# Kernel optimization log

Measured on AMD Instinct MI355X. Metric: run time of the kernel, lower is better.

The kernel has to match this reference:

```python
import jax, jax.numpy as jnp
import numpy as np

B, T, C, H = 4, 2048, 1024, 16
D = C // H  # head_dim = 64


def setup_inputs() -> dict:
    key = jax.random.key(0)
    ks = jax.random.split(key, 5)
    s = 0.02
    return {
        "x": jax.random.normal(ks[0], (B, T, C), dtype=jnp.float32),
        "w_qkv": jax.random.normal(ks[1], (C, 3 * C), dtype=jnp.float32) * s,
        "b_qkv": jnp.zeros((3 * C,), dtype=jnp.float32),
        "w_proj": jax.random.normal(ks[2], (C, C), dtype=jnp.float32) * s,
        "b_proj": jnp.zeros((C,), dtype=jnp.float32),
    }


def reference(x, w_qkv, b_qkv, w_proj, b_proj):
    Bx, Tx, Cx = x.shape
    qkv = x @ w_qkv + b_qkv                      # [B,T,3C]
    q, k, v = jnp.split(qkv, 3, axis=-1)
    # [B,T,C] -> [B,H,T,D]
    q = q.reshape(Bx, Tx, H, D).transpose(0, 2, 1, 3)
    k = k.reshape(Bx, Tx, H, D).transpose(0, 2, 1, 3)
    v = v.reshape(Bx, Tx, H, D).transpose(0, 2, 1, 3)
    scale = 1.0 / np.sqrt(D).astype(np.float32)
    attn = jnp.einsum('bhqd,bhkd->bhqk', q, k) * scale   # [B,H,T,T]
    causal = jnp.tril(jnp.ones((Tx, Tx), dtype=bool))
    attn = jnp.where(causal[None, None], attn, -jnp.inf)
    attn = jax.nn.softmax(attn, axis=-1)
    out = jnp.einsum('bhqk,bhkd->bhqd', attn, v)          # [B,H,T,D]
    out = out.transpose(0, 2, 1, 3).reshape(Bx, Tx, Cx)   # [B,T,C]
    return out @ w_proj + b_proj
```

## Files before the change

kernel.cpp:

```cpp
#include <hip/hip_runtime.h>
#include <hip/hip_bf16.h>
#include <math.h>

using bf16 = __hip_bfloat16;
typedef __bf16 bf16x8 __attribute__((ext_vector_type(8)));
typedef float  f32x4  __attribute__((ext_vector_type(4)));
typedef unsigned short ushort8 __attribute__((ext_vector_type(8)));

#define DEV __device__ __forceinline__

DEV void gld_lds16(const void* g, void* l) {
    __builtin_amdgcn_global_load_lds((const __attribute__((address_space(1))) void*)g,
                                     (__attribute__((address_space(3))) void*)l,
                                     16, 0, 0);
}

__global__ __launch_bounds__(256) void cast_f32_bf16(const float* __restrict__ in,
                                                     bf16* __restrict__ out, int n4) {
    int i = blockIdx.x * blockDim.x + threadIdx.x;
    if (i >= n4) return;
    float4 f = ((const float4*)in)[i];
    __align__(8) bf16 o[4] = {__float2bfloat16(f.x), __float2bfloat16(f.y),
                              __float2bfloat16(f.z), __float2bfloat16(f.w)};
    ((uint64_t*)out)[i] = *(const uint64_t*)o;
}

__global__ __launch_bounds__(256) void transpose_cast(const float* __restrict__ in,
                                                      bf16* __restrict__ out, int R, int Cn) {
    __shared__ float tile[32][33];
    int bx = blockIdx.x * 32;
    int by = blockIdx.y * 32;
    int tx = threadIdx.x & 31, ty = threadIdx.x >> 5;
    for (int i = ty; i < 32; i += 8)
        tile[i][tx] = in[(size_t)(by + i) * Cn + bx + tx];
    __syncthreads();
    for (int i = ty; i < 32; i += 8)
        out[(size_t)(bx + i) * R + by + tx] = __float2bfloat16(tile[tx][i]);
}

__global__ __launch_bounds__(256) void gemm_qkv(const bf16* __restrict__ A,
                                                const bf16* __restrict__ Bt,
                                                const float* __restrict__ bias,
                                                bf16* __restrict__ qb,
                                                bf16* __restrict__ kb,
                                                bf16* __restrict__ vTb) {
    constexpr int K = 1024, T = 2048;
    constexpr float CS = 0.18033688f;
    __shared__ __align__(16) bf16 Al[128 * 32];
    __shared__ __align__(16) bf16 Bl[128 * 32];
    __shared__ __align__(16) bf16 Et[32 * 136];
    int tid = threadIdx.x;
    int lane = tid & 63, w = tid >> 6;
    int wm = w >> 1, wn = w & 1;
    int l15 = lane & 15, quad = lane >> 4;
    int m0 = blockIdx.x * 128, n0 = blockIdx.y * 128;

    f32x4 acc[4][4] = {};
    for (int k0 = 0; k0 < K; k0 += 32) {
        __syncthreads();
        for (int it = 0; it < 2; ++it) {
            int e = (it * 256 + tid) * 8;
            int r = e >> 5, c = e & 31;
            gld_lds16(A  + (size_t)(m0 + r) * K + k0 + c, &Al[e]);
            gld_lds16(Bt + (size_t)(n0 + r) * K + k0 + c, &Bl[e]);
        }
        __syncthreads();
        bf16x8 af[4], bfr[4];
        for (int i = 0; i < 4; ++i)
            af[i] = *(const bf16x8*)&Al[(wm * 64 + i * 16 + l15) * 32 + quad * 8];
        for (int j = 0; j < 4; ++j)
            bfr[j] = *(const bf16x8*)&Bl[(wn * 64 + j * 16 + l15) * 32 + quad * 8];
        for (int i = 0; i < 4; ++i)
            for (int j = 0; j < 4; ++j)
                acc[i][j] = __builtin_amdgcn_mfma_f32_16x16x32_bf16(af[i], bfr[j], acc[i][j], 0, 0, 0);
    }

    int mode = (blockIdx.y < 8) ? 0 : (blockIdx.y < 16 ? 1 : 2);
    float bv[4];
    for (int j = 0; j < 4; ++j)
        bv[j] = bias[n0 + wn * 64 + j * 16 + l15];
    float scl = (mode == 0) ? CS : 1.0f;

    for (int i = 0; i < 4; ++i) {
        __syncthreads();
        for (int j = 0; j < 4; ++j)
            for (int v = 0; v < 4; ++v)
                Et[(wm * 16 + quad * 4 + v) * 136 + wn * 64 + j * 16 + l15] =
                    __float2bfloat16((acc[i][j][v] + bv[j]) * scl);
        __syncthreads();
        if (mode < 2) {
            int r = tid >> 3, cc = (tid & 7) * 16;
            int m = m0 + i * 16 + (r < 16 ? r : r + 48);
            int b = m >> 11, t = m & 2047;
            int n = (n0 & 1023) + cc;
            int h = n >> 6, d = n & 63;
            bf16* dst = (mode == 0 ? qb : kb) + (((size_t)(b * 16 + h)) * T + t) * 64 + d;
            ushort8 u0 = *(const ushort8*)&Et[r * 136 + cc];
            ushort8 u1 = *(const ushort8*)&Et[r * 136 + cc + 8];
            *(ushort8*)dst = u0;
            *(ushort8*)(dst + 8) = u1;
        } else {
            int run = tid >> 7, d = tid & 127;
            int t0 = m0 + i * 16 + run * 64;
            int b = t0 >> 11, tt = t0 & 2047;
            int n = (n0 & 1023) + d;
            int h = n >> 6, dd = n & 63;
            __align__(16) bf16 tmp[16];
            for (int jj = 0; jj < 16; ++jj)
                tmp[jj] = Et[(run * 16 + jj) * 136 + d];
            bf16* dst = vTb + (((size_t)(b * 16 + h)) * 64 + dd) * T + tt;
            *(ushort8*)dst = *(const ushort8*)tmp;
            *(ushort8*)(dst + 8) = *(const ushort8*)(tmp + 8);
        }
    }
}

__global__ __launch_bounds__(256, 4) void flash_attn(const bf16* __restrict__ qb,
                                                     const bf16* __restrict__ kbuf,
                                                     const bf16* __restrict__ vT,
                                                     bf16* __restrict__ ob) {
    constexpr int T = 2048;
    __shared__ __align__(16) bf16 Kl[64 * 64];
    __shared__ __align__(16) bf16 Vl[64 * 64];
    __shared__ __align__(16) bf16 Pl[4 * 2 * 16 * 72];
    int tid = threadIdx.x;
    int lane = tid & 63, w = tid >> 6;
    int l15 = lane & 15, quad = lane >> 4;

    int g = blockIdx.x;
    int quarter = g >> 8;
    int j = (g >> 6) & 3;
    int bh = g & 63;
    int xq;
    switch (quarter) {
        case 0:  xq = 15 - j; break;
        case 1:  xq = 8 + j;  break;
        case 2:  xq = 4 + j;  break;
        default: xq = 3 - j;  break;
    }
    int q0 = xq << 7;
    const bf16* qbase = qb   + (size_t)bh * T * 64;
    const bf16* kbase = kbuf + (size_t)bh * T * 64;
    const bf16* vbase = vT   + (size_t)bh * 64 * T;

    int qg[2];
    bf16x8 qa[2][2];
    for (int s = 0; s < 2; ++s) {
        qg[s] = q0 + w * 32 + s * 16 + l15;
        for (int c = 0; c < 2; ++c)
            qa[s][c] = *(const bf16x8*)(qbase + (size_t)qg[s] * 64 + c * 32 + quad * 8);
    }

    bf16x8 ones;
    for (int i = 0; i < 8; ++i) ones[i] = (__bf16)1.0f;

    f32x4 O[2][4] = {};
    f32x4 O1[2] = {};
    int h7 = l15 & 7;

    int nit = 2 * xq + 2;
    for (int t = 0; t < nit; ++t) {
        int kb = t << 6;
        __syncthreads();
        for (int it = 0; it < 2; ++it) {
            int off = (it * 256 + tid) * 8;
            int r = off >> 6, cb = (off >> 3) & 7;
            gld_lds16(kbase + (size_t)(kb + r) * 64 + ((cb ^ (r & 7)) << 3), &Kl[off]);
            gld_lds16(vbase + (size_t)r * T + kb + ((cb ^ (r & 7)) << 3), &Vl[off]);
        }
        __syncthreads();

        bool maskt = (t >= nit - 2);
        for (int jn = 0; jn < 4; ++jn) {
            int row = jn * 16 + l15;
            bf16x8 a0 = *(const bf16x8*)&Kl[row * 64 + ((quad ^ h7) << 3)];
            bf16x8 a1 = *(const bf16x8*)&Kl[row * 64 + (((4 + quad) ^ h7) << 3)];
            f32x4 sa[2] = {};
            for (int s = 0; s < 2; ++s) {
                sa[s] = __builtin_amdgcn_mfma_f32_16x16x32_bf16(a0, qa[s][0], sa[s], 0, 0, 0);
                sa[s] = __builtin_amdgcn_mfma_f32_16x16x32_bf16(a1, qa[s][1], sa[s], 0, 0, 0);
            }
            for (int s = 0; s < 2; ++s) {
                __align__(8) bf16 pb[4];
                for (int v = 0; v < 4; ++v) {
                    float p = exp2f(sa[s][v]);
                    if (maskt) {
                        int key = kb + jn * 16 + quad * 4 + v;
                        p = (key <= qg[s]) ? p : 0.f;
                    }
                    pb[v] = __float2bfloat16(p);
                }
                *(uint64_t*)&Pl[((w * 2 + s) * 16 + l15) * 72 + jn * 16 + quad * 4] =
                    *(const uint64_t*)pb;
            }
        }
        asm volatile("s_waitcnt lgkmcnt(0)" ::: "memory");
        bf16x8 pf[2][2];
        for (int s = 0; s < 2; ++s) {
            for (int c = 0; c < 2; ++c)
                pf[s][c] = *(const bf16x8*)&Pl[((w * 2 + s) * 16 + l15) * 72 + c * 32 + quad * 8];
            O1[s] = __builtin_amdgcn_mfma_f32_16x16x32_bf16(pf[s][0], ones, O1[s], 0, 0, 0);
            O1[s] = __builtin_amdgcn_mfma_f32_16x16x32_bf16(pf[s][1], ones, O1[s], 0, 0, 0);
        }
        for (int jd = 0; jd < 4; ++jd) {
            int vrow = jd * 16 + l15;
            bf16x8 v0 = *(const bf16x8*)&Vl[vrow * 64 + ((quad ^ h7) << 3)];
            bf16x8 v1 = *(const bf16x8*)&Vl[vrow * 64 + (((4 + quad) ^ h7) << 3)];
            O[0][jd] = __builtin_amdgcn_mfma_f32_16x16x32_bf16(pf[0][0], v0, O[0][jd], 0, 0, 0);
            O[0][jd] = __builtin_amdgcn_mfma_f32_16x16x32_bf16(pf[0][1], v1, O[0][jd], 0, 0, 0);
            O[1][jd] = __builtin_amdgcn_mfma_f32_16x16x32_bf16(pf[1][0], v0, O[1][jd], 0, 0, 0);
            O[1][jd] = __builtin_amdgcn_mfma_f32_16x16x32_bf16(pf[1][1], v1, O[1][jd], 0, 0, 0);
        }
    }

    int b = bh >> 4, h = bh & 15;
    for (int s = 0; s < 2; ++s) {
        float linv[4];
        for (int v = 0; v < 4; ++v) linv[v] = 1.f / O1[s][v];
        for (int jd = 0; jd < 4; ++jd) {
            for (int v = 0; v < 4; ++v) {
                int qr = q0 + w * 32 + s * 16 + quad * 4 + v;
                ob[((size_t)(b * T + qr)) * 1024 + h * 64 + jd * 16 + l15] =
                    __float2bfloat16(O[s][jd][v] * linv[v]);
            }
        }
    }
}

__global__ __launch_bounds__(256) void gemm_proj(const bf16* __restrict__ A,
                                                 const bf16* __restrict__ Bt,
                                                 const float* __restrict__ bias,
                                                 float* __restrict__ out) {
    constexpr int K = 1024, N = 1024;
    __shared__ __align__(16) bf16 Al[128 * 32];
    __shared__ __align__(16) bf16 Bl[128 * 32];
    int tid = threadIdx.x;
    int lane = tid & 63, w = tid >> 6;
    int wm = w >> 1, wn = w & 1;
    int l15 = lane & 15, quad = lane >> 4;
    int m0 = blockIdx.x * 128, n0 = blockIdx.y * 128;

    f32x4 acc[4][4] = {};
    for (int k0 = 0; k0 < K; k0 += 32) {
        __syncthreads();
        for (int it = 0; it < 2; ++it) {
            int e = (it * 256 + tid) * 8;
            int r = e >> 5, c = e & 31;
            gld_lds16(A  + (size_t)(m0 + r) * K + k0 + c, &Al[e]);
            gld_lds16(Bt + (size_t)(n0 + r) * K + k0 + c, &Bl[e]);
        }
        __syncthreads();
        bf16x8 af[4], bfr[4];
        for (int i = 0; i < 4; ++i)
            af[i] = *(const bf16x8*)&Al[(wm * 64 + i * 16 + l15) * 32 + quad * 8];
        for (int j = 0; j < 4; ++j)
            bfr[j] = *(const bf16x8*)&Bl[(wn * 64 + j * 16 + l15) * 32 + quad * 8];
        for (int i = 0; i < 4; ++i)
            for (int j = 0; j < 4; ++j)
                acc[i][j] = __builtin_amdgcn_mfma_f32_16x16x32_bf16(af[i], bfr[j], acc[i][j], 0, 0, 0);
    }
    for (int i = 0; i < 4; ++i) {
        int mbase = m0 + wm * 64 + i * 16 + quad * 4;
        for (int j = 0; j < 4; ++j) {
            int n = n0 + wn * 64 + j * 16 + l15;
            float bv = bias[n];
            for (int v = 0; v < 4; ++v)
                out[(size_t)(mbase + v) * N + n] = acc[i][j][v] + bv;
        }
    }
}

extern "C" void kernel_launch(void* const* d_in, const int* in_sizes, int n_in,
                              void* d_out, int out_size, void* d_ws, size_t ws_size,
                              hipStream_t stream) {
    (void)in_sizes; (void)n_in; (void)out_size; (void)ws_size;
    const float* x      = (const float*)d_in[0];
    const float* w_qkv  = (const float*)d_in[1];
    const float* b_qkv  = (const float*)d_in[2];
    const float* w_proj = (const float*)d_in[3];
    const float* b_proj = (const float*)d_in[4];
    float* out = (float*)d_out;

    char* ws = (char*)d_ws;
    bf16* xb     = (bf16*)(ws);
    bf16* wqkvT  = (bf16*)(ws + (16u << 20));
    bf16* wprojT = (bf16*)(ws + (22u << 20));
    bf16* qbuf   = (bf16*)(ws + (24u << 20));
    bf16* kbuf   = (bf16*)(ws + (40u << 20));
    bf16* vTb    = (bf16*)(ws + (72u << 20));
    bf16* ob     = (bf16*)(ws + (56u << 20));

    cast_f32_bf16<<<8192, 256, 0, stream>>>(x, xb, 8192 * 1024 / 4);
    transpose_cast<<<dim3(3072 / 32, 1024 / 32), 256, 0, stream>>>(w_qkv, wqkvT, 1024, 3072);
    transpose_cast<<<dim3(1024 / 32, 1024 / 32), 256, 0, stream>>>(w_proj, wprojT, 1024, 1024);
    gemm_qkv<<<dim3(64, 24), 256, 0, stream>>>(xb, wqkvT, b_qkv, qbuf, kbuf, vTb);
    flash_attn<<<1024, 256, 0, stream>>>(qbuf, kbuf, vTb, ob);
    gemm_proj<<<dim3(64, 8), 256, 0, stream>>>(ob, wprojT, b_proj, out);
}
```

Before: 258.0 us.

## Double-buffer K tiles and register-prefetch V in flash attention loop

Restructures the attention main loop so the next K tile is loaded into a second LDS buffer via global_load_lds and the next V tile is prefetched into registers, then written to LDS after a barrier at the end of the iteration. This removes one barrier per iteration and overlaps global loads with compute. It also swizzles the P scratch layout instead of padding it, adds s_setprio around MFMA groups, and fully unrolls the inner loops. The cost is extra LDS for the second K buffer and more registers held across the loop, which may reduce occupancy. Correctness depends on the V writes happening only after all waves finish reading Vl, which the added barrier is meant to guarantee.

```diff
diff --git a/kernel.cpp b/kernel.cpp
--- a/kernel.cpp
+++ b/kernel.cpp
@@ -120,9 +120,9 @@
                                                      const bf16* __restrict__ vT,
                                                      bf16* __restrict__ ob) {
     constexpr int T = 2048;
-    __shared__ __align__(16) bf16 Kl[64 * 64];
+    __shared__ __align__(16) bf16 Kl[2][64 * 64];
     __shared__ __align__(16) bf16 Vl[64 * 64];
-    __shared__ __align__(16) bf16 Pl[4 * 2 * 16 * 72];
+    __shared__ __align__(16) bf16 Pl[128 * 64];
     int tid = threadIdx.x;
     int lane = tid & 63, w = tid >> 6;
     int l15 = lane & 15, quad = lane >> 4;
@@ -145,43 +145,69 @@
 
     int qg[2];
     bf16x8 qa[2][2];
+#pragma unroll
     for (int s = 0; s < 2; ++s) {
         qg[s] = q0 + w * 32 + s * 16 + l15;
+#pragma unroll
         for (int c = 0; c < 2; ++c)
             qa[s][c] = *(const bf16x8*)(qbase + (size_t)qg[s] * 64 + c * 32 + quad * 8);
     }
 
     bf16x8 ones;
+#pragma unroll
     for (int i = 0; i < 8; ++i) ones[i] = (__bf16)1.0f;
 
     f32x4 O[2][4] = {};
     f32x4 O1[2] = {};
     int h7 = l15 & 7;
 
+    int off0 = tid * 8, off1 = (256 + tid) * 8;
+    int r0 = off0 >> 6, cb0 = (off0 >> 3) & 7;
+    int r1 = off1 >> 6, cb1 = (off1 >> 3) & 7;
+    int kc0 = (cb0 ^ (r0 & 7)) << 3, kc1 = (cb1 ^ (r1 & 7)) << 3;
+
+    int prow0 = w * 32 + l15;
     int nit = 2 * xq + 2;
+
+    bf16x8 vr0 = *(const bf16x8*)(vbase + (size_t)r0 * T + kc0);
+    bf16x8 vr1 = *(const bf16x8*)(vbase + (size_t)r1 * T + kc1);
+    gld_lds16(kbase + (size_t)r0 * 64 + kc0, &Kl[0][off0]);
+    gld_lds16(kbase + (size_t)r1 * 64 + kc1, &Kl[0][off1]);
+    *(bf16x8*)&Vl[off0] = vr0;
+    *(bf16x8*)&Vl[off1] = vr1;
+
     for (int t = 0; t < nit; ++t) {
+        int cur = t & 1;
+        __syncthreads();
+        bool pre = (t + 1 < nit);
+        if (pre) {
+            int kb2 = (t + 1) << 6, nxt = cur ^ 1;
+            vr0 = *(const bf16x8*)(vbase + (size_t)r0 * T + kb2 + kc0);
+            vr1 = *(const bf16x8*)(vbase + (size_t)r1 * T + kb2 + kc1);
+            gld_lds16(kbase + (size_t)(kb2 + r0) * 64 + kc0, &Kl[nxt][off0]);
+            gld_lds16(kbase + (size_t)(kb2 + r1) * 64 + kc1, &Kl[nxt][off1]);
+        }
         int kb = t << 6;
-        __syncthreads();
-        for (int it = 0; it < 2; ++it) {
-            int off = (it * 256 + tid) * 8;
-            int r = off >> 6, cb = (off >> 3) & 7;
-            gld_lds16(kbase + (size_t)(kb + r) * 64 + ((cb ^ (r & 7)) << 3), &Kl[off]);
-            gld_lds16(vbase + (size_t)r * T + kb + ((cb ^ (r & 7)) << 3), &Vl[off]);
-        }
-        __syncthreads();
-
         bool maskt = (t >= nit - 2);
+
+#pragma unroll
         for (int jn = 0; jn < 4; ++jn) {
             int row = jn * 16 + l15;
-            bf16x8 a0 = *(const bf16x8*)&Kl[row * 64 + ((quad ^ h7) << 3)];
-            bf16x8 a1 = *(const bf16x8*)&Kl[row * 64 + (((4 + quad) ^ h7) << 3)];
+            bf16x8 a0 = *(const bf16x8*)&Kl[cur][row * 64 + ((quad ^ h7) << 3)];
+            bf16x8 a1 = *(const bf16x8*)&Kl[cur][row * 64 + (((4 + quad) ^ h7) << 3)];
             f32x4 sa[2] = {};
-            for (int s = 0; s < 2; ++s) {
-                sa[s] = __builtin_amdgcn_mfma_f32_16x16x32_bf16(a0, qa[s][0], sa[s], 0, 0, 0);
-                sa[s] = __builtin_amdgcn_mfma_f32_16x16x32_bf16(a1, qa[s][1], sa[s], 0, 0, 0);
-            }
+            __builtin_amdgcn_s_setprio(1);
+            sa[0] = __builtin_amdgcn_mfma_f32_16x16x32_bf16(a0, qa[0][0], sa[0], 0, 0, 0);
+            sa[0] = __builtin_amdgcn_mfma_f32_16x16x32_bf16(a1, qa[0][1], sa[0], 0, 0, 0);
+            sa[1] = __builtin_amdgcn_mfma_f32_16x16x32_bf16(a0, qa[1][0], sa[1], 0, 0, 0);
+            sa[1] = __builtin_amdgcn_mfma_f32_16x16x32_bf16(a1, qa[1][1], sa[1], 0, 0, 0);
+            __builtin_amdgcn_s_setprio(0);
+            int ubase = jn * 2 + (quad >> 1);
+            int lowo = (quad & 1) << 2;
+#pragma unroll
             for (int s = 0; s < 2; ++s) {
                 __align__(8) bf16 pb[4];
+#pragma unroll
                 for (int v = 0; v < 4; ++v) {
                     float p = exp2f(sa[s][v]);
                     if (maskt) {
@@ -190,34 +216,58 @@
                     }
                     pb[v] = __float2bfloat16(p);
                 }
-                *(uint64_t*)&Pl[((w * 2 + s) * 16 + l15) * 72 + jn * 16 + quad * 4] =
+                int prow = prow0 + s * 16;
+                *(uint64_t*)&Pl[prow * 64 + ((ubase ^ h7) << 3) + lowo] =
                     *(const uint64_t*)pb;
             }
         }
         asm volatile("s_waitcnt lgkmcnt(0)" ::: "memory");
         bf16x8 pf[2][2];
+#pragma unroll
         for (int s = 0; s < 2; ++s) {
+            int prow = prow0 + s * 16;
+#pragma unroll
             for (int c = 0; c < 2; ++c)
-                pf[s][c] = *(const bf16x8*)&Pl[((w * 2 + s) * 16 + l15) * 72 + c * 32 + quad * 8];
+                pf[s][c] = *(const bf16x8*)&Pl[prow * 64 + (((c * 4 + quad) ^ h7) << 3)];
+        }
+
+        __builtin_amdgcn_s_setprio(1);
+#pragma unroll
+        for (int s = 0; s < 2; ++s) {
             O1[s] = __builtin_amdgcn_mfma_f32_16x16x32_bf16(pf[s][0], ones, O1[s], 0, 0, 0);
             O1[s] = __builtin_amdgcn_mfma_f32_16x16x32_bf16(pf[s][1], ones, O1[s], 0, 0, 0);
         }
+        __builtin_amdgcn_s_setprio(0);
+
+#pragma unroll
         for (int jd = 0; jd < 4; ++jd) {
             int vrow = jd * 16 + l15;
             bf16x8 v0 = *(const bf16x8*)&Vl[vrow * 64 + ((quad ^ h7) << 3)];
             bf16x8 v1 = *(const bf16x8*)&Vl[vrow * 64 + (((4 + quad) ^ h7) << 3)];
+            __builtin_amdgcn_s_setprio(1);
             O[0][jd] = __builtin_amdgcn_mfma_f32_16x16x32_bf16(pf[0][0], v0, O[0][jd], 0, 0, 0);
             O[0][jd] = __builtin_amdgcn_mfma_f32_16x16x32_bf16(pf[0][1], v1, O[0][jd], 0, 0, 0);
             O[1][jd] = __builtin_amdgcn_mfma_f32_16x16x32_bf16(pf[1][0], v0, O[1][jd], 0, 0, 0);
             O[1][jd] = __builtin_amdgcn_mfma_f32_16x16x32_bf16(pf[1][1], v1, O[1][jd], 0, 0, 0);
+            __builtin_amdgcn_s_setprio(0);
+        }
+
+        __builtin_amdgcn_s_barrier();
+        if (pre) {
+            *(bf16x8*)&Vl[off0] = vr0;
+            *(bf16x8*)&Vl[off1] = vr1;
         }
     }
 
     int b = bh >> 4, h = bh & 15;
+#pragma unroll
     for (int s = 0; s < 2; ++s) {
         float linv[4];
+#pragma unroll
         for (int v = 0; v < 4; ++v) linv[v] = 1.f / O1[s][v];
+#pragma unroll
         for (int jd = 0; jd < 4; ++jd) {
+#pragma unroll
             for (int v = 0; v < 4; ++v) {
                 int qr = q0 + w * 32 + s * 16 + quad * 4 + v;
                 ob[((size_t)(b * T + qr)) * 1024 + h * 64 + jd * 16 + l15] =
```

Result: no change. 256.9 us (-0.5%).
